# Kernel tuning notes

Measured on AMD Instinct MI355X. Metric: run time of the kernel, lower is better.

## Reference

```python
import jax, jax.numpy as jnp
import numpy as np

LATENT_DIM = 768

def setup_inputs() -> dict:
    key = jax.random.key(0)
    k1, k2 = jax.random.split(key)
    x_latent = jax.random.normal(k1, (16, 4096, LATENT_DIM), dtype=jnp.float32)
    prompts_latent = jax.random.normal(k2, (16, 64, LATENT_DIM), dtype=jnp.float32)
    return {"x_latent": x_latent, "prompts_latent": prompts_latent}

def reference(x_latent, prompts_latent):
    # Base class: get_tokens / get_query are identity in the base math.
    tokens = x_latent            # [b, n, d]
    q = prompts_latent           # [b, p, d]
    scale = LATENT_DIM ** (-0.5)
    # [b, p, n] scores
    attn = jnp.einsum('bpd,bnd->bpn', q, tokens) * scale
    attn = jax.nn.softmax(attn, axis=-1)
    # [b, p, d] context
    context = jnp.einsum('bpn,bnd->bpd', attn, tokens)
    return context
```

## Files before the change

kernel.cpp:

```cpp
#include <hip/hip_runtime.h>
#include <hip/hip_bf16.h>

#define BB 16
#define PP 64
#define NN 4096
#define DD 768
#define TT 16
#define NTILE 16
#define VROW 772

typedef __attribute__((ext_vector_type(4))) float f32x4;
typedef __attribute__((ext_vector_type(8))) __bf16 bf16x8;
typedef __attribute__((ext_vector_type(2))) __bf16 bf16x2;
typedef __attribute__((ext_vector_type(4))) short s16x4;
typedef __attribute__((ext_vector_type(4))) _Float16 f16x4;

#if __has_builtin(__builtin_amdgcn_mfma_f32_16x16x16bf16_1k)
#define HAVE_K16 1
#define PSTRIDE 20
#else
#define HAVE_K16 0
#define PSTRIDE 40
#endif

__device__ __forceinline__ f32x4 mfma16(bf16x8 a, bf16x8 b, f32x4 c) {
    return __builtin_amdgcn_mfma_f32_16x16x32_bf16(a, b, c, 0, 0, 0);
}

__device__ __forceinline__ void gl_lds(const float* g, float* l) {
    __builtin_amdgcn_global_load_lds(
        (const __attribute__((address_space(1))) void*)g,
        (__attribute__((address_space(3))) void*)l, 16, 0, 0);
}

__device__ __forceinline__ short bf2s(float f) {
    __bf16 h = (__bf16)f;
    return *(short*)&h;
}

#define S_WAITCNT_VM(N) asm volatile("s_waitcnt vmcnt(" #N ")" ::: "memory")
#define BARRIER() do { __builtin_amdgcn_s_barrier(); asm volatile("" ::: "memory"); } while (0)
#define LDS_BARRIER() do { asm volatile("s_waitcnt lgkmcnt(0)" ::: "memory"); \
                           __builtin_amdgcn_s_barrier(); \
                           __builtin_amdgcn_sched_barrier(0); } while (0)

#define SM_BYTES 141568

__global__ __launch_bounds__(512, 2) void k_flash(const float* __restrict__ x,
                                                  const float* __restrict__ q,
                                                  float* __restrict__ statm,
                                                  float* __restrict__ statl,
                                                  _Float16* __restrict__ part) {
    const int b  = blockIdx.x >> 4;
    const int sp = blockIdx.x & 15;
    const int n0 = sp * 256;

    __shared__ __align__(16) char smem[SM_BYTES];
    float*  vst  = (float*)smem;
    float*  lpf  = (float*)(smem + 98816);
    __bf16* pbuf = (__bf16*)(smem + 135680);
    float*  mrun = (float*)(smem + 140800);
    float*  lrun = (float*)(smem + 141056);
    float*  rsc  = (float*)(smem + 141312);

    const int t = threadIdx.x;
    const int w = t >> 6, lane = t & 63;
    const int l15 = lane & 15, hi = lane >> 4;

    const size_t xbase = (size_t)b * NN + n0;
    const size_t qbase = (size_t)b * PP;

    bf16x8 qf[4][3];
    #pragma unroll
    for (int am = 0; am < 4; ++am)
        #pragma unroll
        for (int s = 0; s < 3; ++s) {
            const size_t off = (qbase + am * 16 + l15) * DD + w * 96 + s * 32 + hi * 8;
            const float4 a = *(const float4*)&q[off];
            const float4 c = *(const float4*)&q[off + 4];
            qf[am][s] = (bf16x8){(__bf16)a.x, (__bf16)a.y, (__bf16)a.z, (__bf16)a.w,
                                 (__bf16)c.x, (__bf16)c.y, (__bf16)c.z, (__bf16)c.w};
        }

#if !HAVE_K16
    for (int i = t; i < 64 * PSTRIDE / 2; i += 512) ((unsigned*)pbuf)[i] = 0;
#endif
    if (t < 64) { mrun[t] = -1e30f; lrun[t] = 0.f; }

    f32x4 O[4][6] = {};

#define STAGE(bufi, tile) do {                                                \
        float* vb_ = vst + (bufi) * (TT * VROW);                              \
        _Pragma("unroll")                                                     \
        for (int i_ = 0; i_ < 6; ++i_) {                                      \
            const int idx_ = w * 6 + i_;                                      \
            const int r_ = idx_ / 3, c_ = idx_ % 3;                           \
            gl_lds(&x[(xbase + (size_t)(tile) * TT + r_) * DD + c_ * 256 + lane * 4], \
                   vb_ + r_ * VROW + c_ * 256);                               \
        }                                                                     \
    } while (0)

    STAGE(0, 0);

    const float scale = 0.036084391824351615f;
    const int p_  = t >> 3;
    const int np_ = t & 7;

    for (int tile = 0; tile < NTILE; ++tile) {
        if (tile < NTILE - 1) { STAGE((tile + 1) & 1, tile + 1); S_WAITCNT_VM(6); }
        else                  { S_WAITCNT_VM(0); }
        BARRIER();
        const float* vb = vst + (tile & 1) * (TT * VROW);

        f32x4 acc[4] = {};
        #pragma unroll
        for (int s = 0; s < 3; ++s) {
            const int g0 = w * 24 + s * 8 + hi * 2;
            const float* kp = vb + l15 * VROW + g0 * 4;
            const f32x4 lo = *(const f32x4*)kp;
            const f32x4 hg = *(const f32x4*)(kp + 4);
            const bf16x8 kf = {(__bf16)lo[0], (__bf16)lo[1], (__bf16)lo[2], (__bf16)lo[3],
                               (__bf16)hg[0], (__bf16)hg[1], (__bf16)hg[2], (__bf16)hg[3]};
            #pragma unroll
            for (int am = 0; am < 4; ++am) acc[am] = mfma16(qf[am][s], kf, acc[am]);
        }
        #pragma unroll
        for (int am = 0; am < 4; ++am)
            #pragma unroll
            for (int j = 0; j < 4; ++j)
                lpf[(w * 64 + am * 16 + hi * 4 + j) * 18 + l15] = acc[am][j];
        LDS_BARRIER();

        float s0 = 0.f, s1 = 0.f;
        #pragma unroll
        for (int sl = 0; sl < 8; ++sl) {
            const float2 v2 = *(const float2*)&lpf[(sl * 64 + p_) * 18 + 2 * np_];
            s0 += v2.x; s1 += v2.y;
        }
        s0 *= scale; s1 *= scale;
        float mt = fmaxf(s0, s1);
        mt = fmaxf(mt, __shfl_xor(mt, 1));
        mt = fmaxf(mt, __shfl_xor(mt, 2));
        mt = fmaxf(mt, __shfl_xor(mt, 4));
        const float mo = mrun[p_];
        const float mn = fmaxf(mo, mt);
        const float e0 = __expf(s0 - mn), e1 = __expf(s1 - mn);
        float lsum = e0 + e1;
        lsum += __shfl_xor(lsum, 1);
        lsum += __shfl_xor(lsum, 2);
        lsum += __shfl_xor(lsum, 4);
        *(bf16x2*)&pbuf[p_ * PSTRIDE + 2 * np_] = (bf16x2){(__bf16)e0, (__bf16)e1};
        if (np_ == 0) {
            const float f = __expf(mo - mn);
            lrun[p_] = lrun[p_] * f + lsum;
            mrun[p_] = mn;
            rsc[p_]  = f;
        }
        LDS_BARRIER();

        #pragma unroll
        for (int am = 0; am < 4; ++am)
            #pragma unroll
            for (int j = 0; j < 4; ++j) {
                const float f = rsc[am * 16 + hi * 4 + j];
                #pragma unroll
                for (int df = 0; df < 6; ++df) O[am][df][j] *= f;
            }

#if HAVE_K16
        s16x4 pf[4];
        #pragma unroll
        for (int am = 0; am < 4; ++am)
            pf[am] = *(const s16x4*)&pbuf[(am * 16 + l15) * PSTRIDE + hi * 4];
        #pragma unroll
        for (int df = 0; df < 6; ++df) {
            const int d_ = w * 96 + df * 16 + l15;
            s16x4 vfr;
            #pragma unroll
            for (int i = 0; i < 4; ++i) {
                const int k_ = hi * 4 + i;
                vfr[i] = bf2s(vb[k_ * VROW + d_]);
            }
            #pragma unroll
            for (int am = 0; am < 4; ++am)
                O[am][df] = __builtin_amdgcn_mfma_f32_16x16x16bf16_1k(pf[am], vfr, O[am][df], 0, 0, 0);
        }
#else
        bf16x8 pf[4];
        #pragma unroll
        for (int am = 0; am < 4; ++am)
            pf[am] = *(const bf16x8*)&pbuf[(am * 16 + l15) * PSTRIDE + hi * 8];
        #pragma unroll
        for (int df = 0; df < 6; ++df) {
            const int d_ = w * 96 + df * 16 + l15;
            float vf[8];
            #pragma unroll
            for (int i = 0; i < 8; ++i) {
                const int k_ = (hi * 8 + i) & 15;
                vf[i] = vb[k_ * VROW + d_];
            }
            const bf16x8 vfr = {(__bf16)vf[0], (__bf16)vf[1], (__bf16)vf[2], (__bf16)vf[3],
                                (__bf16)vf[4], (__bf16)vf[5], (__bf16)vf[6], (__bf16)vf[7]};
            #pragma unroll
            for (int am = 0; am < 4; ++am) O[am][df] = mfma16(pf[am], vfr, O[am][df]);
        }
#endif
        LDS_BARRIER();
    }

    if (t < 64) {
        const size_t si = ((size_t)b * 16 + sp) * 64 + t;
        statm[si] = mrun[t];
        statl[si] = lrun[t];
    }
    #pragma unroll
    for (int am = 0; am < 4; ++am)
        #pragma unroll
        for (int j = 0; j < 4; ++j) {
            const int p = am * 16 + hi * 4 + j;
            #pragma unroll
            for (int df = 0; df < 6; ++df) {
                const int d_ = w * 96 + df * 16 + l15;
                part[(((size_t)sp * BB + b) * PP + p) * DD + d_] = (_Float16)O[am][df][j];
            }
        }
}

__global__ __launch_bounds__(256) void k_combine(const _Float16* __restrict__ part,
                                                 const float* __restrict__ statm,
                                                 const float* __restrict__ statl,
                                                 float* __restrict__ out) {
    const size_t idx = (size_t)blockIdx.x * 256 + threadIdx.x;
    const size_t e = idx * 4;
    const int bp = (int)(e / DD);
    const int b = bp >> 6, p = bp & 63;

    float M = -1e30f;
    #pragma unroll
    for (int c = 0; c < 16; ++c) M = fmaxf(M, statm[((size_t)b * 16 + c) * 64 + p]);
    float Ee[16];
    float D = 0.f;
    #pragma unroll
    for (int c = 0; c < 16; ++c) {
        Ee[c] = __expf(statm[((size_t)b * 16 + c) * 64 + p] - M);
        D += Ee[c] * statl[((size_t)b * 16 + c) * 64 + p];
    }
    const float inv = 1.f / D;

    float4 v = {0.f, 0.f, 0.f, 0.f};
    #pragma unroll
    for (int c = 0; c < 16; ++c) {
        const f16x4 h = *(const f16x4*)&part[(size_t)c * ((size_t)BB * PP * DD) + e];
        v.x += Ee[c] * (float)h[0];
        v.y += Ee[c] * (float)h[1];
        v.z += Ee[c] * (float)h[2];
        v.w += Ee[c] * (float)h[3];
    }
    v.x *= inv; v.y *= inv; v.z *= inv; v.w *= inv;
    *(float4*)&out[e] = v;
}

extern "C" void kernel_launch(void* const* d_in, const int* in_sizes, int n_in,
                              void* d_out, int out_size, void* d_ws, size_t ws_size,
                              hipStream_t stream) {
    const float* x = (const float*)d_in[0];
    const float* q = (const float*)d_in[1];
    float* out = (float*)d_out;

    char* ws = (char*)d_ws;
    float*     statm = (float*)ws;
    float*     statl = (float*)(ws + 65536);
    _Float16*  part  = (_Float16*)(ws + 131072);

    hipLaunchKernelGGL(k_flash,   dim3(256), dim3(512), 0, stream, x, q, statm, statl, part);
    hipLaunchKernelGGL(k_combine, dim3(768), dim3(256), 0, stream, part, statm, statl, out);
}
```

Before: 61.81 us.

## Halve KV tile to 8 rows and deepen prefetch to four buffers

Tiles shrink from 16 to 8 token rows, and the kernel switches from double buffering to a 4-deep ring with 3 tiles in flight, using less LDS. The aim is more memory-level parallelism and a smaller shared footprint. The price is half-empty MFMAs (only 8 of 16 columns do useful work, with zeroed P padding) and twice as many barrier-synchronised iterations. It also skips rescaling O when every factor is 1 across the wave.

```diff
diff --git a/kernel.cpp b/kernel.cpp
--- a/kernel.cpp
+++ b/kernel.cpp
@@ -5,13 +5,12 @@
 #define PP 64
 #define NN 4096
 #define DD 768
-#define TT 16
-#define NTILE 16
+#define TT 8
+#define NTILE 32
 #define VROW 772
 
 typedef __attribute__((ext_vector_type(4))) float f32x4;
 typedef __attribute__((ext_vector_type(8))) __bf16 bf16x8;
-typedef __attribute__((ext_vector_type(2))) __bf16 bf16x2;
 typedef __attribute__((ext_vector_type(4))) short s16x4;
 typedef __attribute__((ext_vector_type(4))) _Float16 f16x4;
 
@@ -44,7 +43,7 @@
                            __builtin_amdgcn_s_barrier(); \
                            __builtin_amdgcn_sched_barrier(0); } while (0)
 
-#define SM_BYTES 141568
+#define SM_BYTES 125184
 
 __global__ __launch_bounds__(512, 2) void k_flash(const float* __restrict__ x,
                                                   const float* __restrict__ q,
@@ -58,10 +57,10 @@
     __shared__ __align__(16) char smem[SM_BYTES];
     float*  vst  = (float*)smem;
     float*  lpf  = (float*)(smem + 98816);
-    __bf16* pbuf = (__bf16*)(smem + 135680);
-    float*  mrun = (float*)(smem + 140800);
-    float*  lrun = (float*)(smem + 141056);
-    float*  rsc  = (float*)(smem + 141312);
+    __bf16* pbuf = (__bf16*)(smem + 119296);
+    float*  mrun = (float*)(smem + 124416);
+    float*  lrun = (float*)(smem + 124672);
+    float*  rsc  = (float*)(smem + 124928);
 
     const int t = threadIdx.x;
     const int w = t >> 6, lane = t & 63;
@@ -82,9 +81,7 @@
                                  (__bf16)c.x, (__bf16)c.y, (__bf16)c.z, (__bf16)c.w};
         }
 
-#if !HAVE_K16
     for (int i = t; i < 64 * PSTRIDE / 2; i += 512) ((unsigned*)pbuf)[i] = 0;
-#endif
     if (t < 64) { mrun[t] = -1e30f; lrun[t] = 0.f; }
 
     f32x4 O[4][6] = {};
@@ -92,8 +89,8 @@
 #define STAGE(bufi, tile) do {                                                \
         float* vb_ = vst + (bufi) * (TT * VROW);                              \
         _Pragma("unroll")                                                     \
-        for (int i_ = 0; i_ < 6; ++i_) {                                      \
-            const int idx_ = w * 6 + i_;                                      \
+        for (int i_ = 0; i_ < 3; ++i_) {                                      \
+            const int idx_ = w * 3 + i_;                                      \
             const int r_ = idx_ / 3, c_ = idx_ % 3;                           \
             gl_lds(&x[(xbase + (size_t)(tile) * TT + r_) * DD + c_ * 256 + lane * 4], \
                    vb_ + r_ * VROW + c_ * 256);                               \
@@ -101,22 +98,26 @@
     } while (0)
 
     STAGE(0, 0);
+    STAGE(1, 1);
+    STAGE(2, 2);
 
     const float scale = 0.036084391824351615f;
     const int p_  = t >> 3;
     const int np_ = t & 7;
 
     for (int tile = 0; tile < NTILE; ++tile) {
-        if (tile < NTILE - 1) { STAGE((tile + 1) & 1, tile + 1); S_WAITCNT_VM(6); }
-        else                  { S_WAITCNT_VM(0); }
+        if (tile < NTILE - 3)      { STAGE((tile + 3) & 3, tile + 3); S_WAITCNT_VM(9); }
+        else if (tile == NTILE - 3) { S_WAITCNT_VM(6); }
+        else if (tile == NTILE - 2) { S_WAITCNT_VM(3); }
+        else                        { S_WAITCNT_VM(0); }
         BARRIER();
-        const float* vb = vst + (tile & 1) * (TT * VROW);
+        const float* vb = vst + (tile & 3) * (TT * VROW);
 
         f32x4 acc[4] = {};
         #pragma unroll
         for (int s = 0; s < 3; ++s) {
             const int g0 = w * 24 + s * 8 + hi * 2;
-            const float* kp = vb + l15 * VROW + g0 * 4;
+            const float* kp = vb + (l15 & 7) * VROW + g0 * 4;
             const f32x4 lo = *(const f32x4*)kp;
             const f32x4 hg = *(const f32x4*)(kp + 4);
             const bf16x8 kf = {(__bf16)lo[0], (__bf16)lo[1], (__bf16)lo[2], (__bf16)lo[3],
@@ -124,32 +125,31 @@
             #pragma unroll
             for (int am = 0; am < 4; ++am) acc[am] = mfma16(qf[am][s], kf, acc[am]);
         }
-        #pragma unroll
-        for (int am = 0; am < 4; ++am)
-            #pragma unroll
-            for (int j = 0; j < 4; ++j)
-                lpf[(w * 64 + am * 16 + hi * 4 + j) * 18 + l15] = acc[am][j];
+        if (l15 < 8) {
+            #pragma unroll
+            for (int am = 0; am < 4; ++am)
+                #pragma unroll
+                for (int j = 0; j < 4; ++j)
+                    lpf[(w * 64 + am * 16 + hi * 4 + j) * 10 + l15] = acc[am][j];
+        }
         LDS_BARRIER();
 
-        float s0 = 0.f, s1 = 0.f;
-        #pragma unroll
-        for (int sl = 0; sl < 8; ++sl) {
-            const float2 v2 = *(const float2*)&lpf[(sl * 64 + p_) * 18 + 2 * np_];
-            s0 += v2.x; s1 += v2.y;
-        }
-        s0 *= scale; s1 *= scale;
-        float mt = fmaxf(s0, s1);
+        float s0 = 0.f;
+        #pragma unroll
+        for (int sl = 0; sl < 8; ++sl) s0 += lpf[(sl * 64 + p_) * 10 + np_];
+        s0 *= scale;
+        float mt = s0;
         mt = fmaxf(mt, __shfl_xor(mt, 1));
         mt = fmaxf(mt, __shfl_xor(mt, 2));
         mt = fmaxf(mt, __shfl_xor(mt, 4));
         const float mo = mrun[p_];
         const float mn = fmaxf(mo, mt);
-        const float e0 = __expf(s0 - mn), e1 = __expf(s1 - mn);
-        float lsum = e0 + e1;
+        const float e0 = __expf(s0 - mn);
+        float lsum = e0;
         lsum += __shfl_xor(lsum, 1);
         lsum += __shfl_xor(lsum, 2);
         lsum += __shfl_xor(lsum, 4);
-        *(bf16x2*)&pbuf[p_ * PSTRIDE + 2 * np_] = (bf16x2){(__bf16)e0, (__bf16)e1};
+        pbuf[p_ * PSTRIDE + np_] = (__bf16)e0;
         if (np_ == 0) {
             const float f = __expf(mo - mn);
             lrun[p_] = lrun[p_] * f + lsum;
@@ -159,13 +159,18 @@
         LDS_BARRIER();
 
         #pragma unroll
-        for (int am = 0; am < 4; ++am)
-            #pragma unroll
-            for (int j = 0; j < 4; ++j) {
-                const float f = rsc[am * 16 + hi * 4 + j];
+        for (int am = 0; am < 4; ++am) {
+            float f[4];
+            #pragma unroll
+            for (int j = 0; j < 4; ++j) f[j] = rsc[am * 16 + hi * 4 + j];
+            const bool nz = (f[0] != 1.f) | (f[1] != 1.f) | (f[2] != 1.f) | (f[3] != 1.f);
+            if (__any(nz)) {
                 #pragma unroll
-                for (int df = 0; df < 6; ++df) O[am][df][j] *= f;
-            }
+                for (int df = 0; df < 6; ++df)
+                    #pragma unroll
+                    for (int j = 0; j < 4; ++j) O[am][df][j] *= f[j];
+            }
+        }
 
 #if HAVE_K16
         s16x4 pf[4];
@@ -178,7 +183,7 @@
             s16x4 vfr;
             #pragma unroll
             for (int i = 0; i < 4; ++i) {
-                const int k_ = hi * 4 + i;
+                const int k_ = (hi * 4 + i) & 7;
                 vfr[i] = bf2s(vb[k_ * VROW + d_]);
             }
             #pragma unroll
@@ -196,7 +201,7 @@
             float vf[8];
             #pragma unroll
             for (int i = 0; i < 8; ++i) {
-                const int k_ = (hi * 8 + i) & 15;
+                const int k_ = (hi * 8 + i) & 7;
                 vf[i] = vb[k_ * VROW + d_];
             }
             const bf16x8 vfr = {(__bf16)vf[0], (__bf16)vf[1], (__bf16)vf[2], (__bf16)vf[3],
```

After: 89.57 us. 44.9% more time.

## Deepen x staging to a five-slot half-tile ring and skip unit rescales

Applied to the files above, without the earlier changes.

Replaces the double-buffered 16-row tile staging with a ring of five 8-row half-tile slots, kept two to three half-tiles ahead so more global-to-LDS loads are in flight while the current tile is computed. Row addressing in the QK and PV loops now chooses between the two half-tile slots. It also skips the O accumulator rescale for a 16-row group when every factor in the wave equals one. LDS use grows to about 160 KB, which may limit how many blocks fit per CU, and the rescale check adds a wave vote and a branch.

```diff
diff --git a/kernel.cpp b/kernel.cpp
--- a/kernel.cpp
+++ b/kernel.cpp
@@ -8,6 +8,7 @@
 #define TT 16
 #define NTILE 16
 #define VROW 772
+#define SLOT (8 * VROW)
 
 typedef __attribute__((ext_vector_type(4))) float f32x4;
 typedef __attribute__((ext_vector_type(8))) __bf16 bf16x8;
@@ -44,7 +45,7 @@
                            __builtin_amdgcn_s_barrier(); \
                            __builtin_amdgcn_sched_barrier(0); } while (0)
 
-#define SM_BYTES 141568
+#define SM_BYTES 163712
 
 __global__ __launch_bounds__(512, 2) void k_flash(const float* __restrict__ x,
                                                   const float* __restrict__ q,
@@ -57,11 +58,11 @@
 
     __shared__ __align__(16) char smem[SM_BYTES];
     float*  vst  = (float*)smem;
-    float*  lpf  = (float*)(smem + 98816);
-    __bf16* pbuf = (__bf16*)(smem + 135680);
-    float*  mrun = (float*)(smem + 140800);
-    float*  lrun = (float*)(smem + 141056);
-    float*  rsc  = (float*)(smem + 141312);
+    float*  lpf  = (float*)(smem + 123520);
+    __bf16* pbuf = (__bf16*)(smem + 160384);
+    float*  mrun = (float*)(smem + 162944);
+    float*  lrun = (float*)(smem + 163200);
+    float*  rsc  = (float*)(smem + 163456);
 
     const int t = threadIdx.x;
     const int w = t >> 6, lane = t & 63;
@@ -89,34 +90,41 @@
 
     f32x4 O[4][6] = {};
 
-#define STAGE(bufi, tile) do {                                                \
-        float* vb_ = vst + (bufi) * (TT * VROW);                              \
+#define STAGE_H(h) do {                                                       \
+        float* vb_ = vst + ((h) % 5) * SLOT;                                  \
         _Pragma("unroll")                                                     \
-        for (int i_ = 0; i_ < 6; ++i_) {                                      \
-            const int idx_ = w * 6 + i_;                                      \
-            const int r_ = idx_ / 3, c_ = idx_ % 3;                           \
-            gl_lds(&x[(xbase + (size_t)(tile) * TT + r_) * DD + c_ * 256 + lane * 4], \
-                   vb_ + r_ * VROW + c_ * 256);                               \
+        for (int i_ = 0; i_ < 3; ++i_) {                                      \
+            gl_lds(&x[(xbase + (size_t)(h) * 8 + w) * DD + i_ * 256 + lane * 4], \
+                   vb_ + w * VROW + i_ * 256);                                \
         }                                                                     \
     } while (0)
 
-    STAGE(0, 0);
+    STAGE_H(0); STAGE_H(1); STAGE_H(2);
 
     const float scale = 0.036084391824351615f;
     const int p_  = t >> 3;
     const int np_ = t & 7;
 
     for (int tile = 0; tile < NTILE; ++tile) {
-        if (tile < NTILE - 1) { STAGE((tile + 1) & 1, tile + 1); S_WAITCNT_VM(6); }
-        else                  { S_WAITCNT_VM(0); }
+        if (tile < NTILE - 2) {
+            STAGE_H(2 * tile + 3); STAGE_H(2 * tile + 4);
+            S_WAITCNT_VM(9);
+        } else if (tile == NTILE - 2) {
+            STAGE_H(31);
+            S_WAITCNT_VM(6);
+        } else {
+            S_WAITCNT_VM(0);
+        }
         BARRIER();
-        const float* vb = vst + (tile & 1) * (TT * VROW);
+        const float* vbl = vst + ((2 * tile)     % 5) * SLOT;
+        const float* vbh = vst + ((2 * tile + 1) % 5) * SLOT;
+        const float* rowq = (l15 < 8) ? (vbl + l15 * VROW) : (vbh + (l15 - 8) * VROW);
 
         f32x4 acc[4] = {};
         #pragma unroll
         for (int s = 0; s < 3; ++s) {
             const int g0 = w * 24 + s * 8 + hi * 2;
-            const float* kp = vb + l15 * VROW + g0 * 4;
+            const float* kp = rowq + g0 * 4;
             const f32x4 lo = *(const f32x4*)kp;
             const f32x4 hg = *(const f32x4*)(kp + 4);
             const bf16x8 kf = {(__bf16)lo[0], (__bf16)lo[1], (__bf16)lo[2], (__bf16)lo[3],
@@ -159,15 +167,22 @@
         LDS_BARRIER();
 
         #pragma unroll
-        for (int am = 0; am < 4; ++am)
-            #pragma unroll
-            for (int j = 0; j < 4; ++j) {
-                const float f = rsc[am * 16 + hi * 4 + j];
+        for (int am = 0; am < 4; ++am) {
+            float f[4];
+            #pragma unroll
+            for (int j = 0; j < 4; ++j) f[j] = rsc[am * 16 + hi * 4 + j];
+            const bool nz = (f[0] != 1.f) | (f[1] != 1.f) | (f[2] != 1.f) | (f[3] != 1.f);
+            if (__any(nz)) {
                 #pragma unroll
-                for (int df = 0; df < 6; ++df) O[am][df][j] *= f;
+                for (int df = 0; df < 6; ++df)
+                    #pragma unroll
+                    for (int j = 0; j < 4; ++j) O[am][df][j] *= f[j];
             }
+        }
 
 #if HAVE_K16
+        const float* pvb = (hi < 2) ? (vbl + (hi * 4) * VROW)
+                                    : (vbh + (hi * 4 - 8) * VROW);
         s16x4 pf[4];
         #pragma unroll
         for (int am = 0; am < 4; ++am)
@@ -175,17 +190,16 @@
         #pragma unroll
         for (int df = 0; df < 6; ++df) {
             const int d_ = w * 96 + df * 16 + l15;
+            const float* pvd = pvb + d_;
             s16x4 vfr;
             #pragma unroll
-            for (int i = 0; i < 4; ++i) {
-                const int k_ = hi * 4 + i;
-                vfr[i] = bf2s(vb[k_ * VROW + d_]);
-            }
+            for (int i = 0; i < 4; ++i) vfr[i] = bf2s(pvd[i * VROW]);
             #pragma unroll
             for (int am = 0; am < 4; ++am)
                 O[am][df] = __builtin_amdgcn_mfma_f32_16x16x16bf16_1k(pf[am], vfr, O[am][df], 0, 0, 0);
         }
 #else
+        const float* pvb = (hi & 1) ? vbh : vbl;
         bf16x8 pf[4];
         #pragma unroll
         for (int am = 0; am < 4; ++am)
@@ -193,12 +207,10 @@
         #pragma unroll
         for (int df = 0; df < 6; ++df) {
             const int d_ = w * 96 + df * 16 + l15;
+            const float* pvd = pvb + d_;
             float vf[8];
             #pragma unroll
-            for (int i = 0; i < 8; ++i) {
-                const int k_ = (hi * 8 + i) & 15;
-                vf[i] = vb[k_ * VROW + d_];
-            }
+            for (int i = 0; i < 8; ++i) vf[i] = pvd[i * VROW];
             const bf16x8 vfr = {(__bf16)vf[0], (__bf16)vf[1], (__bf16)vf[2], (__bf16)vf[3],
                                 (__bf16)vf[4], (__bf16)vf[5], (__bf16)vf[6], (__bf16)vf[7]};
             #pragma unroll
```

After: 64.29 us. 4.0% more time.

## Use per-wave XOR-swizzled LDS staging for x tiles and drop tile-level barriers

Applied to the files above, without the earlier changes.

Each wave now stages only its own 96-column slice of the x tile into a private LDS region, using an XOR swizzle on 16-byte groups instead of a padded shared row layout. Because no wave reads another wave's staging region, the barrier at the start and end of each tile iteration is replaced by a local lgkmcnt wait. The rescale of the O accumulators is also skipped when every factor in a wave equals one. The aim is fewer LDS bank conflicts and fewer block-wide synchronisations, at the cost of more complex address arithmetic and reliance on the remaining LDS_BARRIERs to protect the shared lpf/pbuf buffers.

```diff
diff --git a/kernel.cpp b/kernel.cpp
--- a/kernel.cpp
+++ b/kernel.cpp
@@ -7,7 +7,6 @@
 #define DD 768
 #define TT 16
 #define NTILE 16
-#define VROW 772
 
 typedef __attribute__((ext_vector_type(4))) float f32x4;
 typedef __attribute__((ext_vector_type(8))) __bf16 bf16x8;
@@ -17,11 +16,10 @@
 
 #if __has_builtin(__builtin_amdgcn_mfma_f32_16x16x16bf16_1k)
 #define HAVE_K16 1
-#define PSTRIDE 20
 #else
 #define HAVE_K16 0
+#endif
 #define PSTRIDE 40
-#endif
 
 __device__ __forceinline__ f32x4 mfma16(bf16x8 a, bf16x8 b, f32x4 c) {
     return __builtin_amdgcn_mfma_f32_16x16x32_bf16(a, b, c, 0, 0, 0);
@@ -39,12 +37,11 @@
 }
 
 #define S_WAITCNT_VM(N) asm volatile("s_waitcnt vmcnt(" #N ")" ::: "memory")
-#define BARRIER() do { __builtin_amdgcn_s_barrier(); asm volatile("" ::: "memory"); } while (0)
 #define LDS_BARRIER() do { asm volatile("s_waitcnt lgkmcnt(0)" ::: "memory"); \
                            __builtin_amdgcn_s_barrier(); \
                            __builtin_amdgcn_sched_barrier(0); } while (0)
 
-#define SM_BYTES 141568
+#define SM_BYTES 141056
 
 __global__ __launch_bounds__(512, 2) void k_flash(const float* __restrict__ x,
                                                   const float* __restrict__ q,
@@ -57,17 +54,17 @@
 
     __shared__ __align__(16) char smem[SM_BYTES];
     float*  vst  = (float*)smem;
-    float*  lpf  = (float*)(smem + 98816);
-    __bf16* pbuf = (__bf16*)(smem + 135680);
-    float*  mrun = (float*)(smem + 140800);
-    float*  lrun = (float*)(smem + 141056);
-    float*  rsc  = (float*)(smem + 141312);
+    float*  lpf  = (float*)(smem + 98304);
+    __bf16* pbuf = (__bf16*)(smem + 135168);
+    float*  mrun = (float*)(smem + 140288);
+    float*  lrun = (float*)(smem + 140544);
+    float*  rsc  = (float*)(smem + 140800);
 
     const int t = threadIdx.x;
     const int w = t >> 6, lane = t & 63;
     const int l15 = lane & 15, hi = lane >> 4;
 
-    const size_t xbase = (size_t)b * NN + n0;
+    const float* xp = x + ((size_t)b * NN + n0) * DD;
     const size_t qbase = (size_t)b * PP;
 
     bf16x8 qf[4][3];
@@ -86,18 +83,28 @@
     for (int i = t; i < 64 * PSTRIDE / 2; i += 512) ((unsigned*)pbuf)[i] = 0;
 #endif
     if (t < 64) { mrun[t] = -1e30f; lrun[t] = 0.f; }
+#if !HAVE_K16
+    __syncthreads();
+#endif
 
     f32x4 O[4][6] = {};
 
+    int srcF[6];
+    #pragma unroll
+    for (int i = 0; i < 6; ++i) {
+        const int d = i * 64 + lane;
+        const int row  = d / 24;
+        const int slot = d - row * 24;
+        const int g = (slot & ~7) | ((slot & 7) ^ (row & 7));
+        srcF[i] = row * DD + w * 96 + g * 4;
+    }
+
 #define STAGE(bufi, tile) do {                                                \
-        float* vb_ = vst + (bufi) * (TT * VROW);                              \
+        float* vb_ = vst + ((bufi) * 8 + w) * 1536;                           \
+        const float* sp_ = xp + (size_t)(tile) * (TT * DD);                   \
         _Pragma("unroll")                                                     \
-        for (int i_ = 0; i_ < 6; ++i_) {                                      \
-            const int idx_ = w * 6 + i_;                                      \
-            const int r_ = idx_ / 3, c_ = idx_ % 3;                           \
-            gl_lds(&x[(xbase + (size_t)(tile) * TT + r_) * DD + c_ * 256 + lane * 4], \
-                   vb_ + r_ * VROW + c_ * 256);                               \
-        }                                                                     \
+        for (int i_ = 0; i_ < 6; ++i_)                                        \
+            gl_lds(sp_ + srcF[i_], vb_ + i_ * 256);                           \
     } while (0)
 
     STAGE(0, 0);
@@ -107,18 +114,21 @@
     const int np_ = t & 7;
 
     for (int tile = 0; tile < NTILE; ++tile) {
+        asm volatile("s_waitcnt lgkmcnt(0)" ::: "memory");
         if (tile < NTILE - 1) { STAGE((tile + 1) & 1, tile + 1); S_WAITCNT_VM(6); }
         else                  { S_WAITCNT_VM(0); }
-        BARRIER();
-        const float* vb = vst + (tile & 1) * (TT * VROW);
+        __builtin_amdgcn_sched_barrier(0);
+
+        const float* reg = vst + ((tile & 1) * 8 + w) * 1536;
 
         f32x4 acc[4] = {};
         #pragma unroll
         for (int s = 0; s < 3; ++s) {
-            const int g0 = w * 24 + s * 8 + hi * 2;
-            const float* kp = vb + l15 * VROW + g0 * 4;
-            const f32x4 lo = *(const f32x4*)kp;
-            const f32x4 hg = *(const f32x4*)(kp + 4);
+            const int ga = s * 8 + hi * 2, gb = ga + 1;
+            const int sa = (ga & ~7) | ((ga & 7) ^ (l15 & 7));
+            const int sb = (gb & ~7) | ((gb & 7) ^ (l15 & 7));
+            const f32x4 lo = *(const f32x4*)(reg + l15 * 96 + sa * 4);
+            const f32x4 hg = *(const f32x4*)(reg + l15 * 96 + sb * 4);
             const bf16x8 kf = {(__bf16)lo[0], (__bf16)lo[1], (__bf16)lo[2], (__bf16)lo[3],
                                (__bf16)hg[0], (__bf16)hg[1], (__bf16)hg[2], (__bf16)hg[3]};
             #pragma unroll
@@ -159,13 +169,18 @@
         LDS_BARRIER();
 
         #pragma unroll
-        for (int am = 0; am < 4; ++am)
-            #pragma unroll
-            for (int j = 0; j < 4; ++j) {
-                const float f = rsc[am * 16 + hi * 4 + j];
+        for (int am = 0; am < 4; ++am) {
+            float f[4];
+            #pragma unroll
+            for (int j = 0; j < 4; ++j) f[j] = rsc[am * 16 + hi * 4 + j];
+            const bool nz = (f[0] != 1.f) | (f[1] != 1.f) | (f[2] != 1.f) | (f[3] != 1.f);
+            if (__any(nz)) {
                 #pragma unroll
-                for (int df = 0; df < 6; ++df) O[am][df][j] *= f;
-            }
+                for (int df = 0; df < 6; ++df)
+                    #pragma unroll
+                    for (int j = 0; j < 4; ++j) O[am][df][j] *= f[j];
+            }
+        }
 
 #if HAVE_K16
         s16x4 pf[4];
@@ -174,12 +189,14 @@
             pf[am] = *(const s16x4*)&pbuf[(am * 16 + l15) * PSTRIDE + hi * 4];
         #pragma unroll
         for (int df = 0; df < 6; ++df) {
-            const int d_ = w * 96 + df * 16 + l15;
+            const int dl = df * 16 + l15;
+            const int g = dl >> 2, sub = dl & 3;
             s16x4 vfr;
             #pragma unroll
             for (int i = 0; i < 4; ++i) {
-                const int k_ = hi * 4 + i;
-                vfr[i] = bf2s(vb[k_ * VROW + d_]);
+                const int r = hi * 4 + i;
+                const int sl2 = (g & ~7) | ((g & 7) ^ (r & 7));
+                vfr[i] = bf2s(reg[r * 96 + sl2 * 4 + sub]);
             }
             #pragma unroll
             for (int am = 0; am < 4; ++am)
@@ -192,12 +209,14 @@
             pf[am] = *(const bf16x8*)&pbuf[(am * 16 + l15) * PSTRIDE + hi * 8];
         #pragma unroll
         for (int df = 0; df < 6; ++df) {
-            const int d_ = w * 96 + df * 16 + l15;
+            const int dl = df * 16 + l15;
+            const int g = dl >> 2, sub = dl & 3;
             float vf[8];
             #pragma unroll
             for (int i = 0; i < 8; ++i) {
-                const int k_ = (hi * 8 + i) & 15;
-                vf[i] = vb[k_ * VROW + d_];
+                const int r = (hi * 8 + i) & 15;
+                const int sl2 = (g & ~7) | ((g & 7) ^ (r & 7));
+                vf[i] = reg[r * 96 + sl2 * 4 + sub];
             }
             const bf16x8 vfr = {(__bf16)vf[0], (__bf16)vf[1], (__bf16)vf[2], (__bf16)vf[3],
                                 (__bf16)vf[4], (__bf16)vf[5], (__bf16)vf[6], (__bf16)vf[7]};
@@ -205,7 +224,6 @@
             for (int am = 0; am < 4; ++am) O[am][df] = mfma16(pf[am], vfr, O[am][df]);
         }
 #endif
-        LDS_BARRIER();
     }
 
     if (t < 64) {
```

Result: no change. 62.69 us (+1.4%).
